# Performance work log

Measured on AMD Instinct MI355X. Metric: run time of the kernel, lower is better.

The kernel has to match this reference:

```python
import jax, jax.numpy as jnp
import numpy as np

IN_CH = 64
EMBED = 64
STRIDE = 1
F_SCALE = 2

def conv2d(x, w, b, pad, dil):
    y = jax.lax.conv_general_dilated(
        x, w, window_strides=(1, 1),
        padding=((pad, pad), (pad, pad)), rhs_dilation=(dil, dil),
        dimension_numbers=('NCHW', 'OIHW', 'NCHW'))
    return y + b[None, :, None, None]

def layer_norm_chw(x, eps=1e-5):
    # F.layer_norm(x, x.shape[-3:]) : normalize jointly over (C,H,W), no affine
    m = jnp.mean(x, axis=(1, 2, 3), keepdims=True)
    v = jnp.var(x, axis=(1, 2, 3), keepdims=True)
    return (x - m) / jnp.sqrt(v + eps)

def pixel_unshuffle_windows(x, f):
    # matches _pixel_unshuffle + rearrange 'b (f c) h w -> (b f) c h w'
    # (B,c,H,W) -> (B*f*f, c, H/f, W/f), window index k = dh*f + dw (outer)
    B, c, H, W = x.shape
    x = x.reshape(B, c, H // f, f, W // f, f)
    x = x.transpose(0, 3, 5, 1, 2, 4)  # B, dh, dw, c, h, w
    return x.reshape(B * f * f, c, H // f, W // f)

def get_attention(x, unet_output, wqk, convl_w, convl_b, f):
    B, c, H, W = x.shape
    xx = layer_norm_chw(x)
    qk_in = pixel_unshuffle_windows(xx, f)  # (B*f^2, c, sh, sw)
    v_in = pixel_unshuffle_windows(x, f)
    b2, _, sh, sw = qk_in.shape
    n = sh * sw
    qk = qk_in.transpose(0, 2, 3, 1).reshape(b2, n, c)  # (b h w) c ordering
    v = v_in.transpose(0, 2, 3, 1).reshape(b2, n, c)
    qk = qk @ wqk  # (b2, n, EMBED)
    qk = qk / (jnp.linalg.norm(qk, axis=-1, keepdims=True) + 1e-8)
    attn = (jnp.einsum('bne,bme->bnm', qk, qk) + 1.0) / jnp.sqrt(jnp.float32(EMBED))
    attn = jax.nn.softmax(attn, axis=-1)
    out = jnp.einsum('bnm,bmc->bnc', attn, v)
    # faithful raw reshape (as in torch code), not an inverse pixel shuffle
    out = out.reshape(B, -1, H, W)  # (B, c, H, W)
    out = jnp.concatenate([out, unet_output], axis=1)  # (B, 65, H, W)
    return conv2d(out, convl_w, convl_b, 0, 1)

def get_ff(x, c1w, c1b, c2w, c2b, c3w, c3b):
    x = jax.nn.relu(conv2d(x, c1w, c1b, STRIDE, STRIDE))
    x = jax.nn.relu(conv2d(x, c2w, c2b, STRIDE * 2, STRIDE * 2))
    return conv2d(x, c3w, c3b, 0, 1)

def setup_inputs() -> dict:
    key = jax.random.key(0)
    ks = jax.random.split(key, 12)
    B, C, H, W = 1, IN_CH, 128, 128
    s = 0.05
    return {
        'x': jax.random.normal(ks[0], (B, C, H, W), jnp.float32),
        'unet_output': jax.random.normal(ks[1], (B, 1, H, W), jnp.float32),
        'wqk': jax.random.normal(ks[2], (C, EMBED), jnp.float32) * 0.17,  # ~xavier gain 1.414
        'conv1_w': jax.random.normal(ks[3], (C, C, 3, 3), jnp.float32) * s,
        'conv1_b': jax.random.normal(ks[4], (C,), jnp.float32) * s,
        'conv2_w': jax.random.normal(ks[5], (C, C, 3, 3), jnp.float32) * s,
        'conv2_b': jax.random.normal(ks[6], (C,), jnp.float32) * s,
        'conv3_w': jax.random.normal(ks[7], (C, C, 1, 1), jnp.float32) * s,
        'conv3_b': jax.random.normal(ks[8], (C,), jnp.float32) * s,
        'convl_w': jax.random.normal(ks[9], (64, 65, 1, 1), jnp.float32) * s,
        'convl_b': jax.random.normal(ks[10], (64,), jnp.float32) * s,
    }

def reference(x, unet_output, wqk, conv1_w, conv1_b, conv2_w, conv2_b,
              conv3_w, conv3_b, convl_w, convl_b):
    f = F_SCALE * STRIDE
    attn_out = get_attention(x, unet_output, wqk, convl_w, convl_b, f)
    return x + get_ff(x + attn_out, conv1_w, conv1_b, conv2_w, conv2_b, conv3_w, conv3_b)
```

## Files before the change

### kernel.cpp

```cpp
#include <hip/hip_runtime.h>

typedef __bf16 bf16;
typedef bf16 bf16x8 __attribute__((ext_vector_type(8)));
typedef float f32x4 __attribute__((ext_vector_type(4)));

#define MFMA16(a,b,c) __builtin_amdgcn_mfma_f32_16x16x32_bf16(a,b,c,0,0,0)

#define HW 16384
#define NQ 4096

constexpr size_t OFF_RED  = 0;
constexpr size_t OFF_Q    = 4096;
constexpr size_t OFF_QT   = OFF_Q  + (size_t)2097152;
constexpr size_t OFF_VT   = OFF_QT + (size_t)2097152;
constexpr size_t OFF_MP   = OFF_VT + (size_t)2097152;
constexpr size_t OFF_AT   = OFF_MP + (size_t)524288;
constexpr size_t OFF_T    = OFF_AT + (size_t)2097152;
constexpr size_t OFF_T2   = OFF_AT;
constexpr size_t OFF_T3   = OFF_T  + (size_t)2097152;
constexpr size_t OFF_W1   = OFF_T3 + (size_t)2097152;
constexpr size_t OFF_W2   = OFF_W1 + 73728;
constexpr size_t OFF_W3   = OFF_W2 + 73728;
constexpr size_t OFF_WL   = OFF_W3 + 8192;

__global__ __launch_bounds__(256) void k_red1w(const float* __restrict__ x, float* __restrict__ red,
                                               const float* __restrict__ w1, const float* __restrict__ w2,
                                               const float* __restrict__ w3, const float* __restrict__ wlc,
                                               bf16* __restrict__ W1, bf16* __restrict__ W2,
                                               bf16* __restrict__ W3, bf16* __restrict__ WLb) {
    int t = threadIdx.x, bx = blockIdx.x;
    if (bx >= 256) {
        int g = (bx - 256) * 256 + t;
        if (g < 36864) {
            int tap = g >> 12, co = (g >> 6) & 63, ci = g & 63;
            W1[g] = (bf16)w1[(co*64 + ci)*9 + tap];
        } else if (g < 73728) {
            int d = g - 36864;
            int tap = d >> 12, co = (d >> 6) & 63, ci = d & 63;
            W2[d] = (bf16)w2[(co*64 + ci)*9 + tap];
        } else if (g < 77824) {
            int d = g - 73728;
            W3[d] = (bf16)w3[d];
        } else if (g < 81920) {
            int d = g - 77824;
            WLb[d] = (bf16)wlc[(d >> 6)*65 + (d & 63)];
        }
        return;
    }
    float s = 0.f;
    const float* base = x + (size_t)bx*4096;
    #pragma unroll
    for (int k = 0; k < 4; ++k) {
        float4 v = *(const float4*)(base + k*1024 + t*4);
        s += v.x + v.y + v.z + v.w;
    }
    __shared__ float rs[256];
    rs[t] = s; __syncthreads();
    for (int off = 128; off; off >>= 1) {
        if (t < off) rs[t] += rs[t+off];
        __syncthreads();
    }
    if (t == 0) red[bx] = rs[0];
}

__global__ __launch_bounds__(256) void k_qv(const float* __restrict__ x, const float* __restrict__ wqk,
                                            const float* __restrict__ red,
                                            bf16* __restrict__ Q, bf16* __restrict__ Qt,
                                            bf16* __restrict__ Vt) {
    int t = threadIdx.x, bx = blockIdx.x;
    int y = bx >> 2, x0 = (bx & 3) * 32;
    __shared__ float xs[32][65];
    __shared__ float wl[4096];
    __shared__ float rs[256];
    __shared__ float vv[64];
    __shared__ bf16 qts[64][34];

    rs[t] = red[t];
    __syncthreads();
    for (int off = 128; off; off >>= 1) {
        if (t < off) rs[t] += rs[t+off];
        __syncthreads();
    }

    {
        int c = t >> 2, seg = t & 3;
        const float4* xp = (const float4*)(x + (size_t)c*HW + y*128 + x0 + seg*8);
        float f[8];
        float4 v0 = xp[0], v1 = xp[1];
        f[0]=v0.x; f[1]=v0.y; f[2]=v0.z; f[3]=v0.w;
        f[4]=v1.x; f[5]=v1.y; f[6]=v1.z; f[7]=v1.w;
        #pragma unroll
        for (int k = 0; k < 8; ++k) xs[seg*8 + k][c] = f[k];
        int dh = y & 1;
        int base_n = (y >> 1)*64 + ((x0 + seg*8) >> 1);
        bf16* vte = Vt + ((size_t)((dh*2 + 0)*64 + c))*NQ + base_n;
        bf16* vto = Vt + ((size_t)((dh*2 + 1)*64 + c))*NQ + base_n;
        #pragma unroll
        for (int j = 0; j < 4; ++j) { vte[j] = (bf16)f[2*j]; vto[j] = (bf16)f[2*j+1]; }
    }
    {
        const float4* wp = (const float4*)wqk;
        #pragma unroll
        for (int k = 0; k < 4; ++k) {
            float4 v = wp[t*4 + k];
            wl[t*16 + k*4 + 0] = v.x; wl[t*16 + k*4 + 1] = v.y;
            wl[t*16 + k*4 + 2] = v.z; wl[t*16 + k*4 + 3] = v.w;
        }
    }
    __syncthreads();
    if (t < 64) {
        float cs = 0.f;
        for (int c = 0; c < 64; ++c) cs += wl[c*64 + t];
        vv[t] = rs[0] * (1.f/1048576.f) * cs;
    }
    __syncthreads();

    int p = t >> 3, eg = t & 7;
    float acc[8];
    #pragma unroll
    for (int k = 0; k < 8; ++k) acc[k] = 0.f;
    for (int c = 0; c < 64; ++c) {
        float xv = xs[p][c];
        const float* wr = &wl[c*64 + eg*8];
        #pragma unroll
        for (int k = 0; k < 8; ++k) acc[k] += xv * wr[k];
    }
    #pragma unroll
    for (int k = 0; k < 8; ++k) acc[k] -= vv[eg*8 + k];
    float ss = 0.f;
    #pragma unroll
    for (int k = 0; k < 8; ++k) ss += acc[k]*acc[k];
    ss += __shfl_xor(ss, 1);
    ss += __shfl_xor(ss, 2);
    ss += __shfl_xor(ss, 4);
    float inv = 1.f / (sqrtf(ss) + 1e-8f);

    int xp2 = x0 + p;
    int b2 = (y & 1)*2 + (xp2 & 1);
    int nidx = (y >> 1)*64 + (xp2 >> 1);
    bf16x8 qv;
    #pragma unroll
    for (int k = 0; k < 8; ++k) qv[k] = (bf16)(acc[k]*inv);
    *(bf16x8*)(Q + ((size_t)b2*NQ + nidx)*64 + eg*8) = qv;
    #pragma unroll
    for (int k = 0; k < 8; ++k) qts[eg*8 + k][p] = qv[k];
    __syncthreads();

    {
        int e = t >> 2, par = (t >> 1) & 1, seg2 = t & 1;
        int b2w = (y & 1)*2 + par;
        int nbase = (y >> 1)*64 + (x0 >> 1) + seg2*8;
        bf16x8 qt;
        #pragma unroll
        for (int j = 0; j < 8; ++j) qt[j] = qts[e][par + 2*(seg2*8 + j)];
        *(bf16x8*)(Qt + ((size_t)b2w*64 + e)*NQ + nbase) = qt;
    }
}

__global__ __launch_bounds__(320) void k_gemm1(const bf16* __restrict__ Vt, const bf16* __restrict__ Qt,
                                               float* __restrict__ MP) {
    int bx = blockIdx.x;
    int b2 = bx & 3, kc = bx >> 2;
    int tid = threadIdx.x, w = tid >> 6, lane = tid & 63, q = lane >> 4, l15 = lane & 15;
    const bf16* Vb  = Vt + (size_t)b2*64*NQ;
    const bf16* Qtb = Qt + (size_t)b2*64*NQ;
    bf16x8 onesfrag = {};
    if (l15 == 0) {
        #pragma unroll
        for (int k = 0; k < 8; ++k) onesfrag[k] = (bf16)1.0f;
    }
    f32x4 acc[5];
    #pragma unroll
    for (int nt = 0; nt < 5; ++nt) acc[nt] = (f32x4){0.f,0.f,0.f,0.f};

    int k0 = kc*1024 + q*8;
    for (int it = 0; it < 32; ++it) {
        int kk = k0 + it*32;
        bf16x8 a;
        if (w < 4) a = *(const bf16x8*)(Vb + (size_t)(w*16 + l15)*NQ + kk);
        else       a = onesfrag;
        bf16x8 b[5];
        #pragma unroll
        for (int nt = 0; nt < 4; ++nt) b[nt] = *(const bf16x8*)(Qtb + (size_t)(nt*16 + l15)*NQ + kk);
        b[4] = onesfrag;
        #pragma unroll
        for (int nt = 0; nt < 5; ++nt) acc[nt] = MFMA16(a, b[nt], acc[nt]);
    }
    float* mp = MP + (size_t)bx*6400;
    #pragma unroll
    for (int nt = 0; nt < 5; ++nt)
        #pragma unroll
        for (int r = 0; r < 4; ++r)
            mp[(w*16 + q*4 + r)*80 + nt*16 + l15] = acc[nt][r];
}

__global__ __launch_bounds__(256) void k_gemm2(const bf16* __restrict__ Q, const float* __restrict__ MP,
                                               bf16* __restrict__ attn) {
    int bx = blockIdx.x;
    int b2 = bx & 3, nh = bx >> 2;
    int tid = threadIdx.x, w = tid >> 6, lane = tid & 63, q = lane >> 4, l15 = lane & 15;
    __shared__ __align__(16) bf16 Ms[80][80];
    for (int i = tid; i < 6400; i += 256) {
        float s = MP[(size_t)b2*6400 + i] + MP[(size_t)(b2+4)*6400 + i]
                + MP[(size_t)(b2+8)*6400 + i] + MP[(size_t)(b2+12)*6400 + i];
        int rr = i / 80;
        Ms[rr][i - rr*80] = (bf16)s;
    }
    __syncthreads();

    const bf16* Qb = Q + ((size_t)b2*NQ + nh*256 + w*64)*64;
    f32x4 acc[4][5];
    #pragma unroll
    for (int mt = 0; mt < 4; ++mt)
        #pragma unroll
        for (int ct = 0; ct < 5; ++ct) acc[mt][ct] = (f32x4){0.f,0.f,0.f,0.f};

    #pragma unroll
    for (int kt = 0; kt < 2; ++kt) {
        bf16x8 bfr[5];
        #pragma unroll
        for (int ct = 0; ct < 5; ++ct) bfr[ct] = *(const bf16x8*)&Ms[ct*16 + l15][kt*32 + q*8];
        #pragma unroll
        for (int mt = 0; mt < 4; ++mt) {
            bf16x8 a = *(const bf16x8*)(Qb + (size_t)(mt*16 + l15)*64 + kt*32 + q*8);
            #pragma unroll
            for (int ct = 0; ct < 5; ++ct) acc[mt][ct] = MFMA16(a, bfr[ct], acc[mt][ct]);
        }
    }
    float c0v[4];
    #pragma unroll
    for (int ct = 0; ct < 4; ++ct) c0v[ct] = (float)Ms[ct*16 + l15][64];

    bf16* arow = attn + (size_t)(b2*16 + nh)*HW + w*64*64;
    #pragma unroll
    for (int mt = 0; mt < 4; ++mt) {
        #pragma unroll
        for (int r = 0; r < 4; ++r) {
            float ldot = __shfl(acc[mt][4][r], lane & 48);
            float rl = 1.0f / fmaf(ldot, 0.125f, 4096.0f);
            int rr = mt*16 + q*4 + r;
            #pragma unroll
            for (int ct = 0; ct < 4; ++ct) {
                float v = fmaf(acc[mt][ct][r], 0.125f, c0v[ct]) * rl;
                arow[rr*64 + ct*16 + l15] = (bf16)v;
            }
        }
    }
}

__global__ __launch_bounds__(256) void k_convl(const bf16* __restrict__ attn,
                                               const float* __restrict__ unet, const float* __restrict__ x,
                                               const bf16* __restrict__ WLb, const float* __restrict__ wl,
                                               const float* __restrict__ bl, bf16* __restrict__ T) {
    int t = threadIdx.x, bx = blockIdx.x;
    int p0 = bx * 64;
    __shared__ __align__(16) bf16 As[64][72];
    {
        int ci = t >> 2, seg = t & 3;
        const bf16* src = attn + (size_t)ci*HW + p0 + seg*16;
        bf16x8 v0 = *(const bf16x8*)src;
        bf16x8 v1 = *(const bf16x8*)(src + 8);
        #pragma unroll
        for (int k = 0; k < 8; ++k) { As[seg*16 + k][ci] = v0[k]; As[seg*16 + 8 + k][ci] = v1[k]; }
    }
    __syncthreads();

    int w = t >> 6, lane = t & 63, q = lane >> 4, l15 = lane & 15;
    int co = w*16 + l15;
    const bf16* wp = WLb + co*64 + q*8;
    bf16x8 b0 = *(const bf16x8*)wp;
    bf16x8 b1 = *(const bf16x8*)(wp + 32);
    f32x4 z = (f32x4){0.f,0.f,0.f,0.f};
    f32x4 o[4];
    #pragma unroll
    for (int mt = 0; mt < 4; ++mt) {
        bf16x8 a0 = *(const bf16x8*)&As[mt*16 + l15][q*8];
        bf16x8 a1 = *(const bf16x8*)&As[mt*16 + l15][32 + q*8];
        f32x4 s = MFMA16(a0, b0, z);
        o[mt] = MFMA16(a1, b1, s);
    }
    float wlu = wl[co*65 + 64];
    float bias = bl[co];
    #pragma unroll
    for (int mt = 0; mt < 4; ++mt) {
        int pb = p0 + mt*16 + q*4;
        float4 un  = *(const float4*)(unet + pb);
        float4 xs4 = *(const float4*)(x + (size_t)co*HW + pb);
        float xv[4] = {xs4.x, xs4.y, xs4.z, xs4.w};
        float uv[4] = {un.x, un.y, un.z, un.w};
        #pragma unroll
        for (int r = 0; r < 4; ++r) {
            float v = o[mt][r] + uv[r]*wlu + bias + xv[r];
            T[(size_t)(pb + r)*64 + co] = (bf16)v;
        }
    }
}

__global__ __launch_bounds__(256) void k_conv3x3(const bf16* __restrict__ IN, const bf16* __restrict__ WT,
                                                 const float* __restrict__ B, bf16* __restrict__ OUT,
                                                 int dil) {
    int tid = threadIdx.x, bx = blockIdx.x;
    int y = bx >> 3, xh = (bx >> 2) & 1, coq = bx & 3;
    int w = tid >> 6, lane = tid & 63, q = lane >> 4, l15 = lane & 15;
    int xb = xh*64 + w*16;

    __shared__ __align__(16) bf16 wsl[9][16][72];
    for (int i = tid; i < 1152; i += 256) {
        int tap = i >> 7, rem = i & 127, co = rem >> 3, k8 = (rem & 7) * 8;
        *(bf16x8*)&wsl[tap][co][k8] =
            *(const bf16x8*)(WT + (((size_t)(tap*64 + coq*16 + co)) << 6) + k8);
    }
    __syncthreads();

    f32x4 o = (f32x4){0.f,0.f,0.f,0.f};
    #pragma unroll
    for (int ky = 0; ky < 3; ++ky) {
        int yy = y + (ky - 1)*dil;
        bool yok = (yy >= 0) && (yy < 128);
        #pragma unroll
        for (int kx = 0; kx < 3; ++kx) {
            int xx = xb + l15 + (kx - 1)*dil;
            bool ok = yok && (xx >= 0) && (xx < 128);
            bf16x8 alo = {}, ahi = {};
            if (ok) {
                const bf16* ip = IN + (size_t)(yy*128 + xx)*64 + q*8;
                alo = *(const bf16x8*)ip;
                ahi = *(const bf16x8*)(ip + 32);
            }
            int tap = ky*3 + kx;
            bf16x8 blo = *(const bf16x8*)&wsl[tap][l15][q*8];
            bf16x8 bhi = *(const bf16x8*)&wsl[tap][l15][32 + q*8];
            o = MFMA16(alo, blo, o);
            o = MFMA16(ahi, bhi, o);
        }
    }
    int co = coq*16 + l15;
    float bias = B[co];
    #pragma unroll
    for (int r = 0; r < 4; ++r) {
        float v = fmaxf(o[r] + bias, 0.f);
        OUT[(size_t)(y*128 + xb + q*4 + r)*64 + co] = (bf16)v;
    }
}

__global__ __launch_bounds__(256) void k_conv3(const bf16* __restrict__ T3, const bf16* __restrict__ W3,
                                               const float* __restrict__ b3, const float* __restrict__ x,
                                               float* __restrict__ out) {
    int tid = threadIdx.x, bx = blockIdx.x;
    int pg = bx >> 1, coh = bx & 1;
    int w = tid >> 6, lane = tid & 63, q = lane >> 4, l15 = lane & 15;
    int p0 = pg*64 + w*16;
    const bf16* bp = T3 + (size_t)(p0 + l15)*64 + q*8;
    bf16x8 blo = *(const bf16x8*)bp;
    bf16x8 bhi = *(const bf16x8*)(bp + 32);
    f32x4 z = (f32x4){0.f,0.f,0.f,0.f};
    f32x4 o[2];
    #pragma unroll
    for (int mt = 0; mt < 2; ++mt) {
        const bf16* ap = W3 + (size_t)(coh*32 + mt*16 + l15)*64 + q*8;
        bf16x8 alo = *(const bf16x8*)ap;
        bf16x8 ahi = *(const bf16x8*)(ap + 32);
        f32x4 s = MFMA16(alo, blo, z);
        o[mt] = MFMA16(ahi, bhi, s);
    }
    #pragma unroll
    for (int mt = 0; mt < 2; ++mt) {
        #pragma unroll
        for (int r = 0; r < 4; ++r) {
            int co = coh*32 + mt*16 + q*4 + r;
            size_t idx = (size_t)co*HW + p0 + l15;
            out[idx] = x[idx] + b3[co] + o[mt][r];
        }
    }
}

extern "C" void kernel_launch(void* const* d_in, const int* in_sizes, int n_in,
                              void* d_out, int out_size, void* d_ws, size_t ws_size,
                              hipStream_t stream) {
    (void)in_sizes; (void)n_in; (void)out_size; (void)ws_size;
    const float* x    = (const float*)d_in[0];
    const float* unet = (const float*)d_in[1];
    const float* wqk  = (const float*)d_in[2];
    const float* c1w  = (const float*)d_in[3];
    const float* c1b  = (const float*)d_in[4];
    const float* c2w  = (const float*)d_in[5];
    const float* c2b  = (const float*)d_in[6];
    const float* c3w  = (const float*)d_in[7];
    const float* c3b  = (const float*)d_in[8];
    const float* clw  = (const float*)d_in[9];
    const float* clb  = (const float*)d_in[10];
    float* out = (float*)d_out;

    char* ws = (char*)d_ws;
    float* red   = (float*)(ws + OFF_RED);
    bf16*  Q     = (bf16*)(ws + OFF_Q);
    bf16*  Qt    = (bf16*)(ws + OFF_QT);
    bf16*  Vt    = (bf16*)(ws + OFF_VT);
    float* MP    = (float*)(ws + OFF_MP);
    bf16*  attn  = (bf16*)(ws + OFF_AT);
    bf16*  T     = (bf16*)(ws + OFF_T);
    bf16*  T2    = (bf16*)(ws + OFF_T2);
    bf16*  T3    = (bf16*)(ws + OFF_T3);
    bf16*  W1    = (bf16*)(ws + OFF_W1);
    bf16*  W2    = (bf16*)(ws + OFF_W2);
    bf16*  W3    = (bf16*)(ws + OFF_W3);
    bf16*  WLb   = (bf16*)(ws + OFF_WL);

    k_red1w<<<dim3(576), dim3(256), 0, stream>>>(x, red, c1w, c2w, c3w, clw, W1, W2, W3, WLb);
    k_qv<<<dim3(512),    dim3(256), 0, stream>>>(x, wqk, red, Q, Qt, Vt);
    k_gemm1<<<dim3(16),  dim3(320), 0, stream>>>(Vt, Qt, MP);
    k_gemm2<<<dim3(64),  dim3(256), 0, stream>>>(Q, MP, attn);
    k_convl<<<dim3(256), dim3(256), 0, stream>>>(attn, unet, x, WLb, clw, clb, T);
    k_conv3x3<<<dim3(1024), dim3(256), 0, stream>>>(T,  W1, c1b, T2, 1);
    k_conv3x3<<<dim3(1024), dim3(256), 0, stream>>>(T2, W2, c2b, T3, 2);
    k_conv3<<<dim3(512), dim3(256), 0, stream>>>(T3, W3, c3b, x, out);
}
```

Baseline: 151.3 us.

## Fuse attention apply into 1x1 conv, and dilated conv into final conv

The gemm1 partial sums are now accumulated with atomics into a single zero-initialized buffer, and the zeroing is folded into k_qv. The attention-apply GEMM is fused into the convl kernel, which removes the bf16 attn intermediate and one launch. The dilated 3x3 conv is fused with the final 1x1 conv plus residual, which removes the T3 round trip. The cost is that every convl block redundantly converts the full 4x80x80 M matrix into LDS. The conv23 kernel also reads weights straight from global memory without tiling, and the atomics make the accumulation order nondeterministic.

```diff
diff --git a/kernel.cpp b/kernel.cpp
--- a/kernel.cpp
+++ b/kernel.cpp
@@ -2,9 +2,12 @@
 
 typedef __bf16 bf16;
 typedef bf16 bf16x8 __attribute__((ext_vector_type(8)));
+typedef bf16 bf16x4 __attribute__((ext_vector_type(4)));
 typedef float f32x4 __attribute__((ext_vector_type(4)));
 
 #define MFMA16(a,b,c) __builtin_amdgcn_mfma_f32_16x16x32_bf16(a,b,c,0,0,0)
+
+__device__ inline f32x4 zero4() { f32x4 z; z[0]=0.f; z[1]=0.f; z[2]=0.f; z[3]=0.f; return z; }
 
 #define HW 16384
 #define NQ 4096
@@ -13,12 +16,10 @@
 constexpr size_t OFF_Q    = 4096;
 constexpr size_t OFF_QT   = OFF_Q  + (size_t)2097152;
 constexpr size_t OFF_VT   = OFF_QT + (size_t)2097152;
-constexpr size_t OFF_MP   = OFF_VT + (size_t)2097152;
-constexpr size_t OFF_AT   = OFF_MP + (size_t)524288;
-constexpr size_t OFF_T    = OFF_AT + (size_t)2097152;
-constexpr size_t OFF_T2   = OFF_AT;
-constexpr size_t OFF_T3   = OFF_T  + (size_t)2097152;
-constexpr size_t OFF_W1   = OFF_T3 + (size_t)2097152;
+constexpr size_t OFF_MF   = OFF_VT + (size_t)2097152;
+constexpr size_t OFF_T    = OFF_MF + (size_t)131072;
+constexpr size_t OFF_T2   = OFF_T  + (size_t)2097152;
+constexpr size_t OFF_W1   = OFF_T2 + (size_t)2097152;
 constexpr size_t OFF_W2   = OFF_W1 + 73728;
 constexpr size_t OFF_W3   = OFF_W2 + 73728;
 constexpr size_t OFF_WL   = OFF_W3 + 8192;
@@ -66,7 +67,7 @@
 __global__ __launch_bounds__(256) void k_qv(const float* __restrict__ x, const float* __restrict__ wqk,
                                             const float* __restrict__ red,
                                             bf16* __restrict__ Q, bf16* __restrict__ Qt,
-                                            bf16* __restrict__ Vt) {
+                                            bf16* __restrict__ Vt, float* __restrict__ Mf) {
     int t = threadIdx.x, bx = blockIdx.x;
     int y = bx >> 2, x0 = (bx & 3) * 32;
     __shared__ float xs[32][65];
@@ -75,6 +76,14 @@
     __shared__ float vv[64];
     __shared__ bf16 qts[64][34];
 
+    if (bx < 25) {
+        int i = bx*1024 + t*4;
+        if (i < 25600) {
+            float4 z; z.x = 0.f; z.y = 0.f; z.z = 0.f; z.w = 0.f;
+            *(float4*)(Mf + i) = z;
+        }
+    }
+
     rs[t] = red[t];
     __syncthreads();
     for (int off = 128; off; off >>= 1) {
@@ -158,7 +167,7 @@
 }
 
 __global__ __launch_bounds__(320) void k_gemm1(const bf16* __restrict__ Vt, const bf16* __restrict__ Qt,
-                                               float* __restrict__ MP) {
+                                               float* __restrict__ Mf) {
     int bx = blockIdx.x;
     int b2 = bx & 3, kc = bx >> 2;
     int tid = threadIdx.x, w = tid >> 6, lane = tid & 63, q = lane >> 4, l15 = lane & 15;
@@ -171,7 +180,7 @@
     }
     f32x4 acc[5];
     #pragma unroll
-    for (int nt = 0; nt < 5; ++nt) acc[nt] = (f32x4){0.f,0.f,0.f,0.f};
+    for (int nt = 0; nt < 5; ++nt) acc[nt] = zero4();
 
     int k0 = kc*1024 + q*8;
     for (int it = 0; it < 32; ++it) {
@@ -186,97 +195,72 @@
         #pragma unroll
         for (int nt = 0; nt < 5; ++nt) acc[nt] = MFMA16(a, b[nt], acc[nt]);
     }
-    float* mp = MP + (size_t)bx*6400;
+    float* mp = Mf + (size_t)b2*6400;
     #pragma unroll
     for (int nt = 0; nt < 5; ++nt)
         #pragma unroll
         for (int r = 0; r < 4; ++r)
-            mp[(w*16 + q*4 + r)*80 + nt*16 + l15] = acc[nt][r];
-}
-
-__global__ __launch_bounds__(256) void k_gemm2(const bf16* __restrict__ Q, const float* __restrict__ MP,
-                                               bf16* __restrict__ attn) {
-    int bx = blockIdx.x;
-    int b2 = bx & 3, nh = bx >> 2;
-    int tid = threadIdx.x, w = tid >> 6, lane = tid & 63, q = lane >> 4, l15 = lane & 15;
-    __shared__ __align__(16) bf16 Ms[80][80];
-    for (int i = tid; i < 6400; i += 256) {
-        float s = MP[(size_t)b2*6400 + i] + MP[(size_t)(b2+4)*6400 + i]
-                + MP[(size_t)(b2+8)*6400 + i] + MP[(size_t)(b2+12)*6400 + i];
-        int rr = i / 80;
-        Ms[rr][i - rr*80] = (bf16)s;
-    }
-    __syncthreads();
-
-    const bf16* Qb = Q + ((size_t)b2*NQ + nh*256 + w*64)*64;
-    f32x4 acc[4][5];
-    #pragma unroll
-    for (int mt = 0; mt < 4; ++mt)
-        #pragma unroll
-        for (int ct = 0; ct < 5; ++ct) acc[mt][ct] = (f32x4){0.f,0.f,0.f,0.f};
-
-    #pragma unroll
-    for (int kt = 0; kt < 2; ++kt) {
-        bf16x8 bfr[5];
-        #pragma unroll
-        for (int ct = 0; ct < 5; ++ct) bfr[ct] = *(const bf16x8*)&Ms[ct*16 + l15][kt*32 + q*8];
-        #pragma unroll
-        for (int mt = 0; mt < 4; ++mt) {
-            bf16x8 a = *(const bf16x8*)(Qb + (size_t)(mt*16 + l15)*64 + kt*32 + q*8);
-            #pragma unroll
-            for (int ct = 0; ct < 5; ++ct) acc[mt][ct] = MFMA16(a, bfr[ct], acc[mt][ct]);
-        }
-    }
-    float c0v[4];
-    #pragma unroll
-    for (int ct = 0; ct < 4; ++ct) c0v[ct] = (float)Ms[ct*16 + l15][64];
-
-    bf16* arow = attn + (size_t)(b2*16 + nh)*HW + w*64*64;
-    #pragma unroll
-    for (int mt = 0; mt < 4; ++mt) {
-        #pragma unroll
-        for (int r = 0; r < 4; ++r) {
-            float ldot = __shfl(acc[mt][4][r], lane & 48);
-            float rl = 1.0f / fmaf(ldot, 0.125f, 4096.0f);
-            int rr = mt*16 + q*4 + r;
-            #pragma unroll
-            for (int ct = 0; ct < 4; ++ct) {
-                float v = fmaf(acc[mt][ct][r], 0.125f, c0v[ct]) * rl;
-                arow[rr*64 + ct*16 + l15] = (bf16)v;
-            }
-        }
-    }
-}
-
-__global__ __launch_bounds__(256) void k_convl(const bf16* __restrict__ attn,
-                                               const float* __restrict__ unet, const float* __restrict__ x,
-                                               const bf16* __restrict__ WLb, const float* __restrict__ wl,
-                                               const float* __restrict__ bl, bf16* __restrict__ T) {
+            unsafeAtomicAdd(&mp[(w*16 + q*4 + r)*80 + nt*16 + l15], acc[nt][r]);
+}
+
+__global__ __launch_bounds__(256) void k_g2convl(const bf16* __restrict__ Q, const float* __restrict__ Mf,
+                                                 const float* __restrict__ unet, const float* __restrict__ x,
+                                                 const bf16* __restrict__ WLb, const float* __restrict__ wl,
+                                                 const float* __restrict__ bl, bf16* __restrict__ T) {
     int t = threadIdx.x, bx = blockIdx.x;
     int p0 = bx * 64;
+    __shared__ __align__(16) bf16 Msl[4][80][88];
     __shared__ __align__(16) bf16 As[64][72];
+
+    #pragma unroll
+    for (int ii = 0; ii < 25; ++ii) {
+        int i = ii*1024 + t*4;
+        float4 v = *(const float4*)(Mf + i);
+        int b2i = i / 6400, rem = i - b2i*6400;
+        int rr = rem / 80, cc = rem - rr*80;
+        bf16x4 pk; pk[0] = (bf16)v.x; pk[1] = (bf16)v.y; pk[2] = (bf16)v.z; pk[3] = (bf16)v.w;
+        *(bf16x4*)&Msl[b2i][rr][cc] = pk;
+    }
+    __syncthreads();
+
+    int w = t >> 6, lane = t & 63, q = lane >> 4, l15 = lane & 15;
     {
-        int ci = t >> 2, seg = t & 3;
-        const bf16* src = attn + (size_t)ci*HW + p0 + seg*16;
-        bf16x8 v0 = *(const bf16x8*)src;
-        bf16x8 v1 = *(const bf16x8*)(src + 8);
-        #pragma unroll
-        for (int k = 0; k < 8; ++k) { As[seg*16 + k][ci] = v0[k]; As[seg*16 + 8 + k][ci] = v1[k]; }
-    }
-    __syncthreads();
-
-    int w = t >> 6, lane = t & 63, q = lane >> 4, l15 = lane & 15;
+        int b2 = w;
+        const bf16* qp = Q + ((size_t)b2*NQ + l15*256 + bx)*64 + q*8;
+        bf16x8 a0 = *(const bf16x8*)qp;
+        bf16x8 a1 = *(const bf16x8*)(qp + 32);
+        f32x4 acc[5];
+        #pragma unroll
+        for (int ct = 0; ct < 5; ++ct) {
+            bf16x8 bf0 = *(const bf16x8*)&Msl[b2][ct*16 + l15][q*8];
+            bf16x8 bf1 = *(const bf16x8*)&Msl[b2][ct*16 + l15][32 + q*8];
+            f32x4 s = MFMA16(a0, bf0, zero4());
+            acc[ct] = MFMA16(a1, bf1, s);
+        }
+        float c0v[4];
+        #pragma unroll
+        for (int ct = 0; ct < 4; ++ct) c0v[ct] = (float)Msl[b2][ct*16 + l15][64];
+        #pragma unroll
+        for (int r = 0; r < 4; ++r) {
+            float ldot = __shfl(acc[4][r], lane & 48);
+            float rl = 1.0f / fmaf(ldot, 0.125f, 4096.0f);
+            #pragma unroll
+            for (int ct = 0; ct < 4; ++ct)
+                As[ct*16 + l15][b2*16 + q*4 + r] = (bf16)(fmaf(acc[ct][r], 0.125f, c0v[ct]) * rl);
+        }
+    }
+    __syncthreads();
+
     int co = w*16 + l15;
     const bf16* wp = WLb + co*64 + q*8;
     bf16x8 b0 = *(const bf16x8*)wp;
     bf16x8 b1 = *(const bf16x8*)(wp + 32);
-    f32x4 z = (f32x4){0.f,0.f,0.f,0.f};
     f32x4 o[4];
     #pragma unroll
     for (int mt = 0; mt < 4; ++mt) {
         bf16x8 a0 = *(const bf16x8*)&As[mt*16 + l15][q*8];
         bf16x8 a1 = *(const bf16x8*)&As[mt*16 + l15][32 + q*8];
-        f32x4 s = MFMA16(a0, b0, z);
+        f32x4 s = MFMA16(a0, b0, zero4());
         o[mt] = MFMA16(a1, b1, s);
     }
     float wlu = wl[co*65 + 64];
@@ -312,7 +296,7 @@
     }
     __syncthreads();
 
-    f32x4 o = (f32x4){0.f,0.f,0.f,0.f};
+    f32x4 o = zero4();
     #pragma unroll
     for (int ky = 0; ky < 3; ++ky) {
         int yy = y + (ky - 1)*dil;
@@ -343,33 +327,75 @@
     }
 }
 
-__global__ __launch_bounds__(256) void k_conv3(const bf16* __restrict__ T3, const bf16* __restrict__ W3,
-                                               const float* __restrict__ b3, const float* __restrict__ x,
-                                               float* __restrict__ out) {
+__global__ __launch_bounds__(256) void k_conv23(const bf16* __restrict__ IN, const bf16* __restrict__ W2T,
+                                                const float* __restrict__ b2v, const bf16* __restrict__ W3,
+                                                const float* __restrict__ b3, const float* __restrict__ x,
+                                                float* __restrict__ out) {
     int tid = threadIdx.x, bx = blockIdx.x;
-    int pg = bx >> 1, coh = bx & 1;
+    int y = bx >> 2, xq = bx & 3;
     int w = tid >> 6, lane = tid & 63, q = lane >> 4, l15 = lane & 15;
-    int p0 = pg*64 + w*16;
-    const bf16* bp = T3 + (size_t)(p0 + l15)*64 + q*8;
-    bf16x8 blo = *(const bf16x8*)bp;
-    bf16x8 bhi = *(const bf16x8*)(bp + 32);
-    f32x4 z = (f32x4){0.f,0.f,0.f,0.f};
+    int pxg = w & 1, coh = w >> 1;
+    int xb = xq*32 + pxg*16;
+
+    __shared__ __align__(16) bf16 As[32][72];
+
     f32x4 o[2];
+    o[0] = zero4();
+    o[1] = zero4();
+    #pragma unroll
+    for (int ky = 0; ky < 3; ++ky) {
+        int yy = y + (ky - 1)*2;
+        bool yok = (yy >= 0) && (yy < 128);
+        #pragma unroll
+        for (int kx = 0; kx < 3; ++kx) {
+            int xx = xb + l15 + (kx - 1)*2;
+            bool ok = yok && (xx >= 0) && (xx < 128);
+            bf16x8 alo = {}, ahi = {};
+            if (ok) {
+                const bf16* ip = IN + (size_t)(yy*128 + xx)*64 + q*8;
+                alo = *(const bf16x8*)ip;
+                ahi = *(const bf16x8*)(ip + 32);
+            }
+            int tap = ky*3 + kx;
+            #pragma unroll
+            for (int ct = 0; ct < 2; ++ct) {
+                const bf16* wp = W2T + (size_t)(tap*64 + coh*32 + ct*16 + l15)*64 + q*8;
+                bf16x8 blo = *(const bf16x8*)wp;
+                bf16x8 bhi = *(const bf16x8*)(wp + 32);
+                o[ct] = MFMA16(alo, blo, o[ct]);
+                o[ct] = MFMA16(ahi, bhi, o[ct]);
+            }
+        }
+    }
+    #pragma unroll
+    for (int ct = 0; ct < 2; ++ct) {
+        int co = coh*32 + ct*16 + l15;
+        float bias = b2v[co];
+        #pragma unroll
+        for (int r = 0; r < 4; ++r)
+            As[pxg*16 + q*4 + r][co] = (bf16)fmaxf(o[ct][r] + bias, 0.f);
+    }
+    __syncthreads();
+
+    bf16x8 blo = *(const bf16x8*)&As[pxg*16 + l15][q*8];
+    bf16x8 bhi = *(const bf16x8*)&As[pxg*16 + l15][32 + q*8];
+    f32x4 o3[2];
     #pragma unroll
     for (int mt = 0; mt < 2; ++mt) {
         const bf16* ap = W3 + (size_t)(coh*32 + mt*16 + l15)*64 + q*8;
         bf16x8 alo = *(const bf16x8*)ap;
         bf16x8 ahi = *(const bf16x8*)(ap + 32);
-        f32x4 s = MFMA16(alo, blo, z);
-        o[mt] = MFMA16(ahi, bhi, s);
-    }
+        f32x4 s = MFMA16(alo, blo, zero4());
+        o3[mt] = MFMA16(ahi, bhi, s);
+    }
+    int pbase = y*128 + xq*32 + pxg*16 + l15;
     #pragma unroll
     for (int mt = 0; mt < 2; ++mt) {
         #pragma unroll
         for (int r = 0; r < 4; ++r) {
             int co = coh*32 + mt*16 + q*4 + r;
-            size_t idx = (size_t)co*HW + p0 + l15;
-            out[idx] = x[idx] + b3[co] + o[mt][r];
+            size_t idx = (size_t)co*HW + pbase;
+            out[idx] = x[idx] + b3[co] + o3[mt][r];
         }
     }
 }
@@ -396,22 +422,18 @@
     bf16*  Q     = (bf16*)(ws + OFF_Q);
     bf16*  Qt    = (bf16*)(ws + OFF_QT);
     bf16*  Vt    = (bf16*)(ws + OFF_VT);
-    float* MP    = (float*)(ws + OFF_MP);
-    bf16*  attn  = (bf16*)(ws + OFF_AT);
+    float* Mf    = (float*)(ws + OFF_MF);
     bf16*  T     = (bf16*)(ws + OFF_T);
     bf16*  T2    = (bf16*)(ws + OFF_T2);
-    bf16*  T3    = (bf16*)(ws + OFF_T3);
     bf16*  W1    = (bf16*)(ws + OFF_W1);
     bf16*  W2    = (bf16*)(ws + OFF_W2);
     bf16*  W3    = (bf16*)(ws + OFF_W3);
     bf16*  WLb   = (bf16*)(ws + OFF_WL);
 
     k_red1w<<<dim3(576), dim3(256), 0, stream>>>(x, red, c1w, c2w, c3w, clw, W1, W2, W3, WLb);
-    k_qv<<<dim3(512),    dim3(256), 0, stream>>>(x, wqk, red, Q, Qt, Vt);
-    k_gemm1<<<dim3(16),  dim3(320), 0, stream>>>(Vt, Qt, MP);
-    k_gemm2<<<dim3(64),  dim3(256), 0, stream>>>(Q, MP, attn);
-    k_convl<<<dim3(256), dim3(256), 0, stream>>>(attn, unet, x, WLb, clw, clb, T);
-    k_conv3x3<<<dim3(1024), dim3(256), 0, stream>>>(T,  W1, c1b, T2, 1);
-    k_conv3x3<<<dim3(1024), dim3(256), 0, stream>>>(T2, W2, c2b, T3, 2);
-    k_conv3<<<dim3(512), dim3(256), 0, stream>>>(T3, W3, c3b, x, out);
-}
+    k_qv<<<dim3(512),    dim3(256), 0, stream>>>(x, wqk, red, Q, Qt, Vt, Mf);
+    k_gemm1<<<dim3(16),  dim3(320), 0, stream>>>(Vt, Qt, Mf);
+    k_g2convl<<<dim3(256), dim3(256), 0, stream>>>(Q, Mf, unet, x, WLb, clw, clb, T);
+    k_conv3x3<<<dim3(1024), dim3(256), 0, stream>>>(T, W1, c1b, T2, 1);
+    k_conv23<<<dim3(512), dim3(256), 0, stream>>>(T2, W2, c2b, W3, c3b, x, out);
+}
```

After: 144.5 us. -4.5%, faster.
